# Optimization experiments

Measured on AMD Instinct MI355X. Metric: run time of the kernel, lower is better.

The kernel has to match this reference:

```python
import jax, jax.numpy as jnp
import numpy as np

QMAX = 127.0  # int8 symmetric

def fake_quant(x):
    # per-tensor symmetric int8 fake quantization with dynamic absmax scale
    s = jnp.max(jnp.abs(x)) / QMAX + 1e-8
    q = jnp.clip(jnp.round(x / s), -QMAX, QMAX) * s
    return q

def qlinear(x, w, b):
    # QuantLinear: fake-quant activation and weight, then dense
    return jnp.einsum('bnc,oc->bno', fake_quant(x), fake_quant(w)) + b

def qlayernorm(x, g, b, eps=1e-6):
    mu = jnp.mean(x, axis=-1, keepdims=True)
    var = jnp.var(x, axis=-1, keepdims=True)
    y = (x - mu) * jax.lax.rsqrt(var + eps) * g + b
    return fake_quant(y)

def setup_inputs() -> dict:
    key = jax.random.key(0)
    ks = jax.random.split(key, 8)
    B, N, C, H = 32, 577, 768, 3072
    inp = {
        'x': jax.random.normal(ks[0], (B, N, C), jnp.float32),
        'ln1_g': jnp.ones((C,), jnp.float32),
        'ln1_b': jnp.zeros((C,), jnp.float32),
        'qkv_w': jax.random.normal(ks[1], (3 * C, C), jnp.float32) * 0.02,
        'qkv_b': jnp.zeros((3 * C,), jnp.float32),
        'proj_w': jax.random.normal(ks[2], (C, C), jnp.float32) * 0.02,
        'proj_b': jnp.zeros((C,), jnp.float32),
        'ln2_g': jnp.ones((C,), jnp.float32),
        'ln2_b': jnp.zeros((C,), jnp.float32),
        'fc1_w': jax.random.normal(ks[3], (H, C), jnp.float32) * 0.02,
        'fc1_b': jnp.zeros((H,), jnp.float32),
        'fc2_w': jax.random.normal(ks[4], (C, H), jnp.float32) * 0.02,
        'fc2_b': jnp.zeros((C,), jnp.float32),
    }
    return inp

def reference(x, ln1_g, ln1_b, qkv_w, qkv_b, proj_w, proj_b, ln2_g, ln2_b, fc1_w, fc1_b, fc2_w, fc2_b):
    B, N, C = x.shape
    num_heads, head_dim = 12, 64
    scale = head_dim ** -0.5
    # attention branch
    xn = qlayernorm(x, ln1_g, ln1_b)
    qkv = qlinear(xn, qkv_w, qkv_b)                       # [B,N,3C]
    qkv = qkv.reshape(B, N, 3, num_heads, head_dim)
    qkv = jnp.transpose(qkv, (2, 0, 3, 1, 4))             # [3,B,h,N,d]
    q, k, v = qkv[0], qkv[1], qkv[2]
    attn = jnp.einsum('bhnd,bhmd->bhnm', q, k) * scale    # [B,h,N,N]
    attn = jax.nn.softmax(attn, axis=-1)
    xa = jnp.einsum('bhnm,bhmd->bhnd', attn, v)           # [B,h,N,d]
    xa = jnp.transpose(xa, (0, 2, 1, 3)).reshape(B, N, C)
    xa = qlinear(xa, proj_w, proj_b)
    x = x + xa
    # mlp branch
    xn = qlayernorm(x, ln2_g, ln2_b)
    h = qlinear(xn, fc1_w, fc1_b)
    h = jax.nn.gelu(h, approximate=False)
    h = qlinear(h, fc2_w, fc2_b)
    return x + h
```

## Files before the change

kernel.cpp:

```cpp
#include <hip/hip_runtime.h>
#include <hip/hip_bf16.h>
#include <math.h>

#define QMAX 127.0f


typedef unsigned short ushortx8 __attribute__((ext_vector_type(8)));
typedef short bf16x8 __attribute__((ext_vector_type(8)));
typedef float f32x4 __attribute__((ext_vector_type(4)));
typedef int int32x4 __attribute__((ext_vector_type(4)));

__device__ inline float bf2f(unsigned short u) {
    return __uint_as_float(((unsigned int)u) << 16);
}
__device__ inline unsigned short f2bf(float f) {
    __hip_bfloat16 h = __float2bfloat16(f);
    return *reinterpret_cast<unsigned short*>(&h);
}

__device__ inline float gelu_fast(float v) {
    float z = v * 0.70710678118654752f;
    float a = fabsf(z);
    float t = __builtin_amdgcn_rcpf(fmaf(0.3275911f, a, 1.0f));
    float poly = t * fmaf(t, fmaf(t, fmaf(t, fmaf(t, 1.061405429f, -1.453152027f),
                       1.421413741f), -0.284496736f), 0.254829592f);
    float e = exp2f(-a * a * 1.44269504088896340736f);
    float erfa = 1.0f - poly * e;
    float erfz = (z < 0.f) ? -erfa : erfa;
    return 0.5f * v * (1.0f + erfz);
}

__device__ inline void gload16(const char* g, char* l) {
    __builtin_amdgcn_global_load_lds(
        (const __attribute__((address_space(1))) unsigned int*)g,
        (__attribute__((address_space(3))) unsigned int*)l, 16, 0, 0);
}

__device__ inline int xcd_swizzle(int orig, int nwg) {
    int q = nwg >> 3, r = nwg & 7;
    int x = orig & 7, pos = orig >> 3;
    return (x < r ? x * (q + 1) : r * (q + 1) + (x - r) * q) + pos;
}

__global__ void init_slots(unsigned int* am) {
    if (threadIdx.x < 16) am[threadIdx.x] = 0u;
}

__global__ __launch_bounds__(256) void absmax_f32(
    const float* __restrict__ p, size_t n, unsigned int* __restrict__ slot)
{
    float lmax = 0.f;
    for (size_t i = (size_t)blockIdx.x*256 + threadIdx.x; i < n; i += (size_t)gridDim.x*256)
        lmax = fmaxf(lmax, fabsf(p[i]));
    __shared__ float rs[256];
    int t = threadIdx.x;
    rs[t] = lmax; __syncthreads();
    for (int o = 128; o; o >>= 1) {
        if (t < o) rs[t] = fmaxf(rs[t], rs[t+o]);
        __syncthreads();
    }
    if (t == 0) atomicMax(slot, __float_as_uint(rs[0]));
}

__global__ __launch_bounds__(256) void quant_w(
    const float* __restrict__ w, char* __restrict__ q, size_t n,
    const unsigned int* __restrict__ slot)
{
    float s = __uint_as_float(*slot) / QMAX + 1e-8f;
    for (size_t i = (size_t)blockIdx.x*256 + threadIdx.x; i < n; i += (size_t)gridDim.x*256) {
        float k = fminf(fmaxf(rintf(w[i] / s), -QMAX), QMAX);
        q[i] = (char)(int)k;
    }
}

__global__ __launch_bounds__(256) void quant_bf2i8(
    const unsigned short* __restrict__ src, char* __restrict__ dst, size_t n8,
    const unsigned int* __restrict__ slot)
{
    float s  = __uint_as_float(*slot) / QMAX + 1e-8f;
    float rs = 1.0f / s;
    for (size_t i = (size_t)blockIdx.x*256 + threadIdx.x; i < n8; i += (size_t)gridDim.x*256) {
        ushortx8 u = *reinterpret_cast<const ushortx8*>(src + i*8);
        int lo = 0, hi = 0;
        #pragma unroll
        for (int j = 0; j < 4; ++j) {
            int k = (int)fminf(fmaxf(rintf(bf2f(u[j]) * rs), -QMAX), QMAX);
            lo |= (k & 0xff) << (8*j);
        }
        #pragma unroll
        for (int j = 0; j < 4; ++j) {
            int k = (int)fminf(fmaxf(rintf(bf2f(u[4+j]) * rs), -QMAX), QMAX);
            hi |= (k & 0xff) << (8*j);
        }
        reinterpret_cast<int2*>(dst)[i] = make_int2(lo, hi);
    }
}

__global__ __launch_bounds__(256) void ln_absmax(
    const float* __restrict__ x, const float* __restrict__ g, const float* __restrict__ bia,
    int nrows, unsigned int* __restrict__ slot)
{
    const int lane = threadIdx.x & 63;
    const int wv   = threadIdx.x >> 6;
    int wid = blockIdx.x*4 + wv;
    int nw  = gridDim.x*4;
    const float4* g4 = reinterpret_cast<const float4*>(g);
    const float4* b4 = reinterpret_cast<const float4*>(bia);
    float4 ga = g4[lane], gb = g4[lane+64], gc = g4[lane+128];
    float4 ba = b4[lane], bb = b4[lane+64], bc = b4[lane+128];
    float wmax = 0.f;
    for (int row = wid; row < nrows; row += nw) {
        const float4* xr = reinterpret_cast<const float4*>(x + (size_t)row*768);
        float4 xa = xr[lane], xb = xr[lane+64], xc = xr[lane+128];
        float s  = xa.x+xa.y+xa.z+xa.w + xb.x+xb.y+xb.z+xb.w + xc.x+xc.y+xc.z+xc.w;
        float ss = xa.x*xa.x+xa.y*xa.y+xa.z*xa.z+xa.w*xa.w
                 + xb.x*xb.x+xb.y*xb.y+xb.z*xb.z+xb.w*xb.w
                 + xc.x*xc.x+xc.y*xc.y+xc.z*xc.z+xc.w*xc.w;
        #pragma unroll
        for (int off = 32; off; off >>= 1) {
            s  += __shfl_xor(s,  off);
            ss += __shfl_xor(ss, off);
        }
        float mean = s * (1.0f/768.0f);
        float inv  = rsqrtf(ss * (1.0f/768.0f) - mean*mean + 1e-6f);
        float m = 0.f;
        m = fmaxf(m, fabsf((xa.x-mean)*inv*ga.x + ba.x));
        m = fmaxf(m, fabsf((xa.y-mean)*inv*ga.y + ba.y));
        m = fmaxf(m, fabsf((xa.z-mean)*inv*ga.z + ba.z));
        m = fmaxf(m, fabsf((xa.w-mean)*inv*ga.w + ba.w));
        m = fmaxf(m, fabsf((xb.x-mean)*inv*gb.x + bb.x));
        m = fmaxf(m, fabsf((xb.y-mean)*inv*gb.y + bb.y));
        m = fmaxf(m, fabsf((xb.z-mean)*inv*gb.z + bb.z));
        m = fmaxf(m, fabsf((xb.w-mean)*inv*gb.w + bb.w));
        m = fmaxf(m, fabsf((xc.x-mean)*inv*gc.x + bc.x));
        m = fmaxf(m, fabsf((xc.y-mean)*inv*gc.y + bc.y));
        m = fmaxf(m, fabsf((xc.z-mean)*inv*gc.z + bc.z));
        m = fmaxf(m, fabsf((xc.w-mean)*inv*gc.w + bc.w));
        wmax = fmaxf(wmax, m);
    }
    #pragma unroll
    for (int off = 32; off; off >>= 1)
        wmax = fmaxf(wmax, __shfl_xor(wmax, off));
    __shared__ float red[4];
    if (lane == 0) red[wv] = wmax;
    __syncthreads();
    if (threadIdx.x == 0) {
        float m = fmaxf(fmaxf(red[0], red[1]), fmaxf(red[2], red[3]));
        atomicMax(slot, __float_as_uint(m));
    }
}

__global__ __launch_bounds__(256) void ln_quant(
    const float* __restrict__ x, const float* __restrict__ g, const float* __restrict__ bia,
    int nrows, char* __restrict__ yq, const unsigned int* __restrict__ slot)
{
    const int lane = threadIdx.x & 63;
    const int wv   = threadIdx.x >> 6;
    int wid = blockIdx.x*4 + wv;
    int nw  = gridDim.x*4;
    const float4* g4 = reinterpret_cast<const float4*>(g);
    const float4* b4 = reinterpret_cast<const float4*>(bia);
    float4 ga = g4[lane], gb = g4[lane+64], gc = g4[lane+128];
    float4 ba = b4[lane], bb = b4[lane+64], bc = b4[lane+128];
    float s1 = __uint_as_float(*slot) / QMAX + 1e-8f;
    float r1 = 1.0f / s1;
    for (int row = wid; row < nrows; row += nw) {
        const float4* xr = reinterpret_cast<const float4*>(x + (size_t)row*768);
        float4 xa = xr[lane], xb = xr[lane+64], xc = xr[lane+128];
        float s  = xa.x+xa.y+xa.z+xa.w + xb.x+xb.y+xb.z+xb.w + xc.x+xc.y+xc.z+xc.w;
        float ss = xa.x*xa.x+xa.y*xa.y+xa.z*xa.z+xa.w*xa.w
                 + xb.x*xb.x+xb.y*xb.y+xb.z*xb.z+xb.w*xb.w
                 + xc.x*xc.x+xc.y*xc.y+xc.z*xc.z+xc.w*xc.w;
        #pragma unroll
        for (int off = 32; off; off >>= 1) {
            s  += __shfl_xor(s,  off);
            ss += __shfl_xor(ss, off);
        }
        float mean = s * (1.0f/768.0f);
        float inv  = rsqrtf(ss * (1.0f/768.0f) - mean*mean + 1e-6f);
        int* yr = reinterpret_cast<int*>(yq + (size_t)row*768);
        float y0, y1, y2, y3;
        int p;
        y0 = (xa.x-mean)*inv*ga.x + ba.x; y1 = (xa.y-mean)*inv*ga.y + ba.y;
        y2 = (xa.z-mean)*inv*ga.z + ba.z; y3 = (xa.w-mean)*inv*ga.w + ba.w;
        p  = ((int)fminf(fmaxf(rintf(y0*r1), -QMAX), QMAX) & 0xff)
           | (((int)fminf(fmaxf(rintf(y1*r1), -QMAX), QMAX) & 0xff) << 8)
           | (((int)fminf(fmaxf(rintf(y2*r1), -QMAX), QMAX) & 0xff) << 16)
           | (((int)fminf(fmaxf(rintf(y3*r1), -QMAX), QMAX) & 0xff) << 24);
        yr[lane] = p;
        y0 = (xb.x-mean)*inv*gb.x + bb.x; y1 = (xb.y-mean)*inv*gb.y + bb.y;
        y2 = (xb.z-mean)*inv*gb.z + bb.z; y3 = (xb.w-mean)*inv*gb.w + bb.w;
        p  = ((int)fminf(fmaxf(rintf(y0*r1), -QMAX), QMAX) & 0xff)
           | (((int)fminf(fmaxf(rintf(y1*r1), -QMAX), QMAX) & 0xff) << 8)
           | (((int)fminf(fmaxf(rintf(y2*r1), -QMAX), QMAX) & 0xff) << 16)
           | (((int)fminf(fmaxf(rintf(y3*r1), -QMAX), QMAX) & 0xff) << 24);
        yr[lane+64] = p;
        y0 = (xc.x-mean)*inv*gc.x + bc.x; y1 = (xc.y-mean)*inv*gc.y + bc.y;
        y2 = (xc.z-mean)*inv*gc.z + bc.z; y3 = (xc.w-mean)*inv*gc.w + bc.w;
        p  = ((int)fminf(fmaxf(rintf(y0*r1), -QMAX), QMAX) & 0xff)
           | (((int)fminf(fmaxf(rintf(y1*r1), -QMAX), QMAX) & 0xff) << 8)
           | (((int)fminf(fmaxf(rintf(y2*r1), -QMAX), QMAX) & 0xff) << 16)
           | (((int)fminf(fmaxf(rintf(y3*r1), -QMAX), QMAX) & 0xff) << 24);
        yr[lane+128] = p;
    }
}

__global__ __launch_bounds__(256) void gemm_i8(
    const char* __restrict__ Alo, const char* __restrict__ Ahi, int split_row,
    const char* __restrict__ Wq,
    const float* __restrict__ bias, const float* __restrict__ residual,
    void* __restrict__ outp, int M, int N, int K,
    const unsigned int* __restrict__ slotA, float epsA,
    const unsigned int* __restrict__ slotW,
    int apply_gelu, int out_bf16, unsigned int* __restrict__ am_slot)
{
    __shared__ __align__(16) char As0[128*64];
    __shared__ __align__(16) char Ws0[128*64];
    __shared__ __align__(16) char As1[128*64];
    __shared__ __align__(16) char Ws1[128*64];
    __shared__ float sred[256];

    float sA  = __uint_as_float(*slotA) / QMAX + epsA;
    float sW  = __uint_as_float(*slotW) / QMAX + 1e-8f;

    const int t    = threadIdx.x;
    const int lane = t & 63;
    const int w    = t >> 6;
    const int wr   = w >> 1;
    const int wc   = w & 1;
    const int lr   = lane & 15;
    const int lk   = lane >> 4;

    const int gx   = gridDim.x;
    const int nwg  = gx * gridDim.y;
    const int wg   = xcd_swizzle(blockIdx.y * gx + blockIdx.x, nwg);
    const int n0   = (wg % gx) * 128;
    const int m0   = (wg / gx) * 128;

    const int rsub = lane >> 2;
    const int csub = (lane & 3) * 16;

    int32x4 acc[4][4];
    #pragma unroll
    for (int i = 0; i < 4; ++i)
        #pragma unroll
        for (int j = 0; j < 4; ++j)
            acc[i][j] = (int32x4){0,0,0,0};

    auto STAGE = [&](char* Ab, char* Wb, int kt) {
        #pragma unroll
        for (int c = 0; c < 2; ++c) {
            int row  = w*32 + c*16 + rsub;
            int grow = m0 + row;
            if (grow > M-1) grow = M-1;
            const char* base = (grow < split_row) ? Alo : Ahi;
            gload16(base + (size_t)grow*K + kt + csub, Ab + (size_t)(w*32 + c*16)*64);
        }
        #pragma unroll
        for (int c = 0; c < 2; ++c) {
            int row = w*32 + c*16 + rsub;
            gload16(Wq + (size_t)(n0 + row)*K + kt + csub, Wb + (size_t)(w*32 + c*16)*64);
        }
    };
    auto COMPUTE = [&](const char* Ab, const char* Wb) {
        int32x4 af[4], bw[4];
        #pragma unroll
        for (int mi = 0; mi < 4; ++mi)
            af[mi] = *reinterpret_cast<const int32x4*>(
                &Ab[(wr*64 + mi*16 + lr)*64 + lk*16]);
        #pragma unroll
        for (int ni = 0; ni < 4; ++ni)
            bw[ni] = *reinterpret_cast<const int32x4*>(
                &Wb[(wc*64 + ni*16 + lr)*64 + lk*16]);
        #pragma unroll
        for (int mi = 0; mi < 4; ++mi)
            #pragma unroll
            for (int ni = 0; ni < 4; ++ni)
                acc[mi][ni] = __builtin_amdgcn_mfma_i32_16x16x64_i8(
                    af[mi], bw[ni], acc[mi][ni], 0, 0, 0);
    };

    const int nk = K >> 6;
    STAGE(As0, Ws0, 0);
    for (int kt = 0; kt < nk; kt += 2) {
        STAGE(As1, Ws1, (kt+1) << 6);
        asm volatile("s_waitcnt vmcnt(4)" ::: "memory");
        __builtin_amdgcn_sched_barrier(0);
        __builtin_amdgcn_s_barrier();
        COMPUTE(As0, Ws0);
        __builtin_amdgcn_s_barrier();
        if (kt + 2 < nk) {
            STAGE(As0, Ws0, (kt+2) << 6);
            asm volatile("s_waitcnt vmcnt(4)" ::: "memory");
        } else {
            asm volatile("s_waitcnt vmcnt(0)" ::: "memory");
        }
        __builtin_amdgcn_sched_barrier(0);
        __builtin_amdgcn_s_barrier();
        COMPUTE(As1, Ws1);
        __builtin_amdgcn_s_barrier();
    }

    float scale = sA * sW;
    float lmax = 0.f;
    #pragma unroll
    for (int mi = 0; mi < 4; ++mi) {
        #pragma unroll
        for (int j = 0; j < 4; ++j) {
            int m = m0 + wr*64 + mi*16 + lk*4 + j;
            if (m >= M) continue;
            #pragma unroll
            for (int ni = 0; ni < 4; ++ni) {
                int n = n0 + wc*64 + ni*16 + lr;
                float v = scale * (float)acc[mi][ni][j] + bias[n];
                if (residual) v += residual[(size_t)m*N + n];
                if (apply_gelu) v = gelu_fast(v);
                if (out_bf16) {
                    unsigned short ub = f2bf(v);
                    ((unsigned short*)outp)[(size_t)m*N + n] = ub;
                    lmax = fmaxf(lmax, fabsf(bf2f(ub)));
                } else {
                    ((float*)outp)[(size_t)m*N + n] = v;
                    lmax = fmaxf(lmax, fabsf(v));
                }
            }
        }
    }
    if (am_slot) {
        sred[t] = lmax; __syncthreads();
        for (int o = 128; o; o >>= 1) {
            if (t < o) sred[t] = fmaxf(sred[t], sred[t+o]);
            __syncthreads();
        }
        if (t == 0) atomicMax(am_slot, __float_as_uint(sred[0]));
    }
}

__global__ __launch_bounds__(512) void attn_mfma(
    const unsigned short* __restrict__ qkv, unsigned short* __restrict__ xa,
    unsigned int* __restrict__ am_slot)
{
    const int Nn = 577;
    const float SCL2 = 0.125f * 1.44269504088896340736f;
    const int gx = gridDim.x;
    const int wg = xcd_swizzle(blockIdx.y * gx + blockIdx.x, gx * gridDim.y);
    const int q0 = (wg % gx) * 128;
    const int bh = wg / gx;
    const int h  = bh % 12;
    const int b  = bh / 12;
    const int t  = threadIdx.x;
    const int w    = t >> 6;
    const int lane = t & 63;
    const int lr   = lane & 15;
    const int lk   = lane >> 4;

    __shared__ __align__(16) unsigned short Ks[64][72];
    __shared__ __align__(16) unsigned short Vt[64][72];
    __shared__ __align__(16) unsigned short Pw[8][16][72];
    __shared__ float red8[8];

    const size_t rowstride = 2304;
    const size_t basebh = ((size_t)b * Nn) * rowstride + (size_t)h * 64;

    bf16x8 qf[2];
    {
        int row = q0 + w*16 + lr;
        if (row < Nn) {
            const unsigned short* qrow = qkv + (size_t)row * rowstride + basebh;
            qf[0] = *reinterpret_cast<const bf16x8*>(qrow + lk*8);
            qf[1] = *reinterpret_cast<const bf16x8*>(qrow + 32 + lk*8);
        } else {
            #pragma unroll
            for (int j = 0; j < 8; ++j) { qf[0][j] = 0; qf[1][j] = 0; }
        }
    }

    float m_run = -INFINITY, l_run = 0.f;
    f32x4 acc_o[4];
    #pragma unroll
    for (int df = 0; df < 4; ++df) acc_o[df] = (f32x4){0.f,0.f,0.f,0.f};

    for (int kt = 0; kt < 10; ++kt) {
        __syncthreads();
        {
            int r   = t >> 3;
            int e8  = (t & 7) * 8;
            int key = kt*64 + r;
            ushortx8 ku, vu;
            if (key < Nn) {
                const unsigned short* krow = qkv + (size_t)key * rowstride + basebh;
                ku = *reinterpret_cast<const ushortx8*>(krow + 768  + e8);
                vu = *reinterpret_cast<const ushortx8*>(krow + 1536 + e8);
            } else {
                #pragma unroll
                for (int j = 0; j < 8; ++j) { ku[j] = 0; vu[j] = 0; }
            }
            *reinterpret_cast<ushortx8*>(&Ks[r][e8]) = ku;
            int colp = ((((r >> 3) ^ (t & 7)) << 3) | (r & 7));
            #pragma unroll
            for (int j = 0; j < 8; ++j) Vt[e8 + j][colp] = vu[j];
        }
        __syncthreads();

        f32x4 st[4];
        #pragma unroll
        for (int kf = 0; kf < 4; ++kf) st[kf] = (f32x4){0.f,0.f,0.f,0.f};
        __builtin_amdgcn_s_setprio(1);
        #pragma unroll
        for (int kk = 0; kk < 2; ++kk) {
            #pragma unroll
            for (int kf = 0; kf < 4; ++kf) {
                bf16x8 kfrag = *reinterpret_cast<const bf16x8*>(
                    &Ks[kf*16 + lr][kk*32 + lk*8]);
                st[kf] = __builtin_amdgcn_mfma_f32_16x16x32_bf16(
                    kfrag, qf[kk], st[kf], 0, 0, 0);
            }
        }
        __builtin_amdgcn_s_setprio(0);
        #pragma unroll
        for (int kf = 0; kf < 4; ++kf)
            #pragma unroll
            for (int j = 0; j < 4; ++j) {
                int key = kt*64 + kf*16 + lk*4 + j;
                st[kf][j] = (key < Nn) ? st[kf][j] * SCL2 : -INFINITY;
            }

        float tm = st[0][0];
        #pragma unroll
        for (int kf = 0; kf < 4; ++kf)
            #pragma unroll
            for (int j = 0; j < 4; ++j)
                tm = fmaxf(tm, st[kf][j]);
        tm = fmaxf(tm, __shfl_xor(tm, 16));
        tm = fmaxf(tm, __shfl_xor(tm, 32));

        if (__any(tm > m_run + 8.0f)) {
            float nm  = fmaxf(m_run, tm);
            float fac = exp2f(m_run - nm);
            m_run = nm;
            l_run *= fac;
            float facR[4];
            #pragma unroll
            for (int j = 0; j < 4; ++j)
                facR[j] = __shfl(fac, lk*4 + j);
            #pragma unroll
            for (int df = 0; df < 4; ++df)
                #pragma unroll
                for (int j = 0; j < 4; ++j)
                    acc_o[df][j] *= facR[j];
        }

        float ps = 0.f;
        #pragma unroll
        for (int kf = 0; kf < 4; ++kf)
            #pragma unroll
            for (int j = 0; j < 4; ++j) {
                float p = exp2f(st[kf][j] - m_run);
                st[kf][j] = p;
                ps += p;
            }
        ps += __shfl_xor(ps, 16);
        ps += __shfl_xor(ps, 32);
        l_run += ps;

        #pragma unroll
        for (int kf = 0; kf < 4; ++kf)
            #pragma unroll
            for (int j = 0; j < 4; ++j)
                Pw[w][lr][kf*16 + lk*4 + j] = f2bf(st[kf][j]);

        __builtin_amdgcn_s_setprio(1);
        #pragma unroll
        for (int kk = 0; kk < 2; ++kk) {
            bf16x8 pf = *reinterpret_cast<const bf16x8*>(
                &Pw[w][lr][kk*32 + lk*8]);
            #pragma unroll
            for (int df = 0; df < 4; ++df) {
                int ar = df*2 + (lr >> 3);
                bf16x8 vf = *reinterpret_cast<const bf16x8*>(
                    &Vt[df*16 + lr][(((kk*4 + lk) ^ ar) << 3)]);
                acc_o[df] = __builtin_amdgcn_mfma_f32_16x16x32_bf16(
                    pf, vf, acc_o[df], 0, 0, 0);
            }
        }
        __builtin_amdgcn_s_setprio(0);
    }

    float lrow[4];
    #pragma unroll
    for (int j = 0; j < 4; ++j)
        lrow[j] = __shfl(l_run, lk*4 + j);
    float lmax = 0.f;
    #pragma unroll
    for (int j = 0; j < 4; ++j) {
        int m = q0 + w*16 + lk*4 + j;
        if (m < Nn) {
            float rl = 1.0f / lrow[j];
            #pragma unroll
            for (int df = 0; df < 4; ++df) {
                int d = df*16 + lr;
                float o = acc_o[df][j] * rl;
                unsigned short ob = f2bf(o);
                xa[((size_t)(b*Nn + m))*768 + h*64 + d] = ob;
                lmax = fmaxf(lmax, fabsf(bf2f(ob)));
            }
        }
    }
    #pragma unroll
    for (int off = 1; off < 64; off <<= 1)
        lmax = fmaxf(lmax, __shfl_xor(lmax, off));
    if (lane == 0) red8[w] = lmax;
    __syncthreads();
    if (t == 0) {
        float m = 0.f;
        #pragma unroll
        for (int i = 0; i < 8; ++i) m = fmaxf(m, red8[i]);
        atomicMax(am_slot, __float_as_uint(m));
    }
}

extern "C" void kernel_launch(void* const* d_in, const int* in_sizes, int n_in,
                              void* d_out, int out_size, void* d_ws, size_t ws_size,
                              hipStream_t stream)
{
    const float* x      = (const float*)d_in[0];
    const float* ln1_g  = (const float*)d_in[1];
    const float* ln1_b  = (const float*)d_in[2];
    const float* qkv_w  = (const float*)d_in[3];
    const float* qkv_b  = (const float*)d_in[4];
    const float* proj_w = (const float*)d_in[5];
    const float* proj_b = (const float*)d_in[6];
    const float* ln2_g  = (const float*)d_in[7];
    const float* ln2_b  = (const float*)d_in[8];
    const float* fc1_w  = (const float*)d_in[9];
    const float* fc1_b  = (const float*)d_in[10];
    const float* fc2_w  = (const float*)d_in[11];
    const float* fc2_b  = (const float*)d_in[12];
    float* out = (float*)d_out;

    const int B = 32, Nn = 577, C = 768, H3 = 3072;
    const int M = B * Nn;
    const size_t nA = (size_t)M * C;
    const size_t nQ = (size_t)M * 3 * C;
    const size_t nH = (size_t)M * H3;

    const size_t NEEDED = 256 + 2359296 + nA + 2*nH;
    if (ws_size < NEEDED) return;

    char* wsb = (char*)d_ws;
    unsigned int* am = (unsigned int*)wsb;
    char* WQ  = wsb + 256;
    char* XNQ = WQ + 2359296;
    char* BIG = XNQ + nA;
    unsigned short* QKV = (unsigned short*)BIG;
    unsigned short* XA  = (unsigned short*)(BIG + 2*nQ);
    unsigned short* Hbf = (unsigned short*)BIG;
    char* HQ = BIG;

    const int SPLIT = 4608;
    const size_t rowsB = 9216 - 4608, rowsC = 18432 - 9216, rowsD = 18464 - 18432;

    dim3 blk(256);
    int mt128 = (M + 127) / 128;

    init_slots<<<dim3(1), dim3(16), 0, stream>>>(am);

    ln_absmax<<<dim3(2048), blk, 0, stream>>>(x, ln1_g, ln1_b, M, am + 0);
    ln_quant <<<dim3(2048), blk, 0, stream>>>(x, ln1_g, ln1_b, M, XNQ, am + 0);

    absmax_f32<<<dim3(1024), blk, 0, stream>>>(qkv_w, (size_t)3*C*C, am + 6);
    quant_w  <<<dim3(1024), blk, 0, stream>>>(qkv_w, WQ, (size_t)3*C*C, am + 6);
    gemm_i8<<<dim3(3*C/128, mt128), blk, 0, stream>>>(
        XNQ, XNQ, 0, WQ, qkv_b, nullptr, QKV, M, 3*C, C,
        am + 0, 2e-8f, am + 6, 0, 1, nullptr);

    attn_mfma<<<dim3(5, 384), dim3(512), 0, stream>>>(QKV, XA, am + 2);

    quant_bf2i8<<<dim3(2048), blk, 0, stream>>>(XA, XNQ, nA/8, am + 2);

    absmax_f32<<<dim3(1024), blk, 0, stream>>>(proj_w, (size_t)C*C, am + 7);
    quant_w  <<<dim3(1024), blk, 0, stream>>>(proj_w, WQ, (size_t)C*C, am + 7);
    gemm_i8<<<dim3(C/128, mt128), blk, 0, stream>>>(
        XNQ, XNQ, 0, WQ, proj_b, x, out, M, C, C,
        am + 2, 1e-8f, am + 7, 0, 0, nullptr);

    ln_absmax<<<dim3(2048), blk, 0, stream>>>(out, ln2_g, ln2_b, M, am + 4);
    ln_quant <<<dim3(2048), blk, 0, stream>>>(out, ln2_g, ln2_b, M, XNQ, am + 4);

    absmax_f32<<<dim3(1024), blk, 0, stream>>>(fc1_w, (size_t)H3*C, am + 8);
    quant_w  <<<dim3(1024), blk, 0, stream>>>(fc1_w, WQ, (size_t)H3*C, am + 8);
    gemm_i8<<<dim3(H3/128, mt128), blk, 0, stream>>>(
        XNQ, XNQ, 0, WQ, fc1_b, nullptr, Hbf, M, H3, C,
        am + 4, 2e-8f, am + 8, 1, 1, am + 3);

    quant_bf2i8<<<dim3(2048), blk, 0, stream>>>(
        Hbf, XNQ, (size_t)SPLIT*H3/8, am + 3);
    quant_bf2i8<<<dim3(2048), blk, 0, stream>>>(
        Hbf + (size_t)4608*H3, HQ + (size_t)4608*H3, rowsB*H3/8, am + 3);
    quant_bf2i8<<<dim3(2048), blk, 0, stream>>>(
        Hbf + (size_t)9216*H3, HQ + (size_t)9216*H3, rowsC*H3/8, am + 3);
    quant_bf2i8<<<dim3(48),  blk, 0, stream>>>(
        Hbf + (size_t)18432*H3, HQ + (size_t)18432*H3, rowsD*H3/8, am + 3);

    absmax_f32<<<dim3(1024), blk, 0, stream>>>(fc2_w, (size_t)C*H3, am + 9);
    quant_w  <<<dim3(1024), blk, 0, stream>>>(fc2_w, WQ, (size_t)C*H3, am + 9);
    gemm_i8<<<dim3(C/128, mt128), blk, 0, stream>>>(
        XNQ, HQ, SPLIT, WQ, fc2_b, out, out, M, C, H3,
        am + 3, 1e-8f, am + 9, 0, 0, nullptr);
}
```

Baseline: 725.5 us.

## Give each wave private swizzled LDS tiles and drop block barriers in int8 GEMM

```diff
diff --git a/kernel.cpp b/kernel.cpp
--- a/kernel.cpp
+++ b/kernel.cpp
@@ -214,10 +214,8 @@
     const unsigned int* __restrict__ slotW,
     int apply_gelu, int out_bf16, unsigned int* __restrict__ am_slot)
 {
-    __shared__ __align__(16) char As0[128*64];
-    __shared__ __align__(16) char Ws0[128*64];
-    __shared__ __align__(16) char As1[128*64];
-    __shared__ __align__(16) char Ws1[128*64];
+    __shared__ __align__(16) char Abuf[4][2][64*64];
+    __shared__ __align__(16) char Wbuf[4][2][64*64];
     __shared__ float sred[256];
 
     float sA  = __uint_as_float(*slotA) / QMAX + epsA;
@@ -236,9 +234,15 @@
     const int wg   = xcd_swizzle(blockIdx.y * gx + blockIdx.x, nwg);
     const int n0   = (wg % gx) * 128;
     const int m0   = (wg / gx) * 128;
-
-    const int rsub = lane >> 2;
-    const int csub = (lane & 3) * 16;
+    const int tm0  = m0 + wr*64;
+    const int tn0  = n0 + wc*64;
+
+    const int srow = lane >> 2;
+    const int sswz = (lane & 3) ^ ((srow >> 1) & 3);
+    const int rswz = lk ^ ((lr >> 1) & 3);
+
+    char* A0 = Abuf[w][0]; char* A1 = Abuf[w][1];
+    char* W0 = Wbuf[w][0]; char* W1 = Wbuf[w][1];
 
     int32x4 acc[4][4];
     #pragma unroll
@@ -249,29 +253,30 @@
 
     auto STAGE = [&](char* Ab, char* Wb, int kt) {
         #pragma unroll
-        for (int c = 0; c < 2; ++c) {
-            int row  = w*32 + c*16 + rsub;
-            int grow = m0 + row;
-            if (grow > M-1) grow = M-1;
-            const char* base = (grow < split_row) ? Alo : Ahi;
-            gload16(base + (size_t)grow*K + kt + csub, Ab + (size_t)(w*32 + c*16)*64);
-        }
-        #pragma unroll
-        for (int c = 0; c < 2; ++c) {
-            int row = w*32 + c*16 + rsub;
-            gload16(Wq + (size_t)(n0 + row)*K + kt + csub, Wb + (size_t)(w*32 + c*16)*64);
+        for (int c = 0; c < 4; ++c) {
+            int gm = tm0 + c*16 + srow;
+            if (gm > M-1) gm = M-1;
+            const char* base = (gm < split_row) ? Alo : Ahi;
+            gload16(base + (size_t)gm*K + kt + sswz*16, Ab + c*1024);
+        }
+        #pragma unroll
+        for (int c = 0; c < 4; ++c) {
+            int gn = tn0 + c*16 + srow;
+            gload16(Wq + (size_t)gn*K + kt + sswz*16, Wb + c*1024);
         }
     };
-    auto COMPUTE = [&](const char* Ab, const char* Wb) {
-        int32x4 af[4], bw[4];
+    int32x4 af[4], bw[4];
+    auto LOADFRAG = [&](const char* Ab, const char* Wb) {
         #pragma unroll
         for (int mi = 0; mi < 4; ++mi)
             af[mi] = *reinterpret_cast<const int32x4*>(
-                &Ab[(wr*64 + mi*16 + lr)*64 + lk*16]);
+                &Ab[(mi*16 + lr)*64 + rswz*16]);
         #pragma unroll
         for (int ni = 0; ni < 4; ++ni)
             bw[ni] = *reinterpret_cast<const int32x4*>(
-                &Wb[(wc*64 + ni*16 + lr)*64 + lk*16]);
+                &Wb[(ni*16 + lr)*64 + rswz*16]);
+    };
+    auto MFMA = [&]() {
         #pragma unroll
         for (int mi = 0; mi < 4; ++mi)
             #pragma unroll
@@ -281,25 +286,33 @@
     };
 
     const int nk = K >> 6;
-    STAGE(As0, Ws0, 0);
-    for (int kt = 0; kt < nk; kt += 2) {
-        STAGE(As1, Ws1, (kt+1) << 6);
-        asm volatile("s_waitcnt vmcnt(4)" ::: "memory");
+    STAGE(A0, W0, 0);
+    STAGE(A1, W1, 64);
+    int kt = 0;
+    for (; kt < nk - 2; kt += 2) {
+        asm volatile("s_waitcnt vmcnt(8)" ::: "memory");
         __builtin_amdgcn_sched_barrier(0);
-        __builtin_amdgcn_s_barrier();
-        COMPUTE(As0, Ws0);
-        __builtin_amdgcn_s_barrier();
-        if (kt + 2 < nk) {
-            STAGE(As0, Ws0, (kt+2) << 6);
-            asm volatile("s_waitcnt vmcnt(4)" ::: "memory");
-        } else {
-            asm volatile("s_waitcnt vmcnt(0)" ::: "memory");
-        }
+        LOADFRAG(A0, W0);
+        asm volatile("s_waitcnt lgkmcnt(0)" ::: "memory");
         __builtin_amdgcn_sched_barrier(0);
-        __builtin_amdgcn_s_barrier();
-        COMPUTE(As1, Ws1);
-        __builtin_amdgcn_s_barrier();
-    }
+        STAGE(A0, W0, (kt+2) << 6);
+        MFMA();
+        asm volatile("s_waitcnt vmcnt(8)" ::: "memory");
+        __builtin_amdgcn_sched_barrier(0);
+        LOADFRAG(A1, W1);
+        asm volatile("s_waitcnt lgkmcnt(0)" ::: "memory");
+        __builtin_amdgcn_sched_barrier(0);
+        STAGE(A1, W1, (kt+3) << 6);
+        MFMA();
+    }
+    asm volatile("s_waitcnt vmcnt(8)" ::: "memory");
+    __builtin_amdgcn_sched_barrier(0);
+    LOADFRAG(A0, W0);
+    MFMA();
+    asm volatile("s_waitcnt vmcnt(0)" ::: "memory");
+    __builtin_amdgcn_sched_barrier(0);
+    LOADFRAG(A1, W1);
+    MFMA();
 
     float scale = sA * sW;
     float lmax = 0.f;
@@ -307,11 +320,11 @@
     for (int mi = 0; mi < 4; ++mi) {
         #pragma unroll
         for (int j = 0; j < 4; ++j) {
-            int m = m0 + wr*64 + mi*16 + lk*4 + j;
+            int m = tm0 + mi*16 + lk*4 + j;
             if (m >= M) continue;
             #pragma unroll
             for (int ni = 0; ni < 4; ++ni) {
-                int n = n0 + wc*64 + ni*16 + lr;
+                int n = tn0 + ni*16 + lr;
                 float v = scale * (float)acc[mi][ni][j] + bias[n];
                 if (residual) v += residual[(size_t)m*N + n];
                 if (apply_gelu) v = gelu_fast(v);
```

New measurement: 811.1 us. 1.12x slower.
